# Kernel tuning notes

Measured on AMD Instinct MI355X. Metric: run time of the kernel, lower is better.

The kernel has to match this reference:

```python
import jax, jax.numpy as jnp
import numpy as np

B, S, H = 2, 512, 768
E, M, R, R2 = 64, 64, 128, 128
NER_C, REL_C, SIZE_E, CLS = 10, 8, 32, 101
NEG = -1e30


def _linear(x, w, b):
    # torch nn.Linear convention: w is [out, in]
    return x @ w.T + b


def _span_pool(emb, masks):
    # emb [B,S,H], masks [B,K,S] -> masked max over tokens -> [B,K,H]
    neg = jnp.where(masks[..., None] != 0, 0.0, NEG)  # [B,K,S,1]
    return jnp.max(neg + emb[:, None, :, :], axis=2)


def _classify_spans(input_ids, emb, masks, size_emb, rep_w, rep_b, head_w, head_b):
    pool = _span_pool(emb, masks)                      # [B,K,H]
    cls_idx = jnp.argmax((input_ids == CLS).astype(jnp.int32), axis=1)
    ctx = emb[jnp.arange(emb.shape[0]), cls_idx]       # [B,H] (get_token)
    rep = jnp.concatenate([jnp.broadcast_to(ctx[:, None, :], pool.shape), pool, size_emb], axis=-1)
    clf = _linear(jax.nn.relu(_linear(rep, rep_w, rep_b)), head_w, head_b)
    return clf, pool


def _classify_relations(pool, size_emb, rels, rel_masks, emb, w1, b1, w2, b2, w3, b3):
    Bc = pool.shape[0]
    bidx = jnp.arange(Bc)[:, None, None]
    pairs = pool[bidx, rels].reshape(Bc, rels.shape[1], -1)        # [B,R,2H]
    size_pairs = size_emb[bidx, rels].reshape(Bc, rels.shape[1], -1)  # [B,R,2*SIZE_E]
    # masked max over context tokens (rel mask)
    ctx = jnp.max(jnp.where(rel_masks[..., None] != 0, 0.0, NEG) + emb[:, None, :, :], axis=2)
    ctx = jnp.where(jnp.any(rel_masks != 0, axis=-1)[..., None], ctx, 0.0)
    rel_repr = jnp.concatenate([ctx, pairs, size_pairs], axis=-1)  # [B,R,3H+2*SIZE_E]
    h = jax.nn.relu(_linear(rel_repr, w1, b1))
    h = jax.nn.relu(_linear(h, w2, b2))
    return _linear(h, w3, b3)


def setup_inputs():
    key = jax.random.key(0)
    ks = jax.random.split(key, 24)
    p = lambda k, shape: jax.random.normal(k, shape, jnp.float32) * 0.02
    ids = jax.random.randint(ks[0], (B, S), 2000, 30000)
    ids = ids.at[:, 0].set(CLS)  # exactly one cls token per row
    return dict(
        input_ids=ids,
        entity_masks=jax.random.randint(ks[1], (B, E, S), 0, 2).astype(jnp.int32),
        entity_sizes=jax.random.randint(ks[2], (B, E), 0, 100),
        mention_masks=jax.random.randint(ks[3], (B, M, S), 0, 2).astype(jnp.int32),
        mention_sizes=jax.random.randint(ks[4], (B, M), 0, 100),
        relations=jax.random.randint(ks[5], (B, R, 2), 0, E),
        rel_masks=jax.random.randint(ks[6], (B, R, S), 0, 2).astype(jnp.int32),
        references=jax.random.randint(ks[7], (B, R2, 2), 0, M),
        references_masks=jax.random.randint(ks[8], (B, R2, S), 0, 2).astype(jnp.int32),
        token_embedding=jax.random.normal(ks[9], (B, S, H), jnp.float32),
        ner_size_emb=p(ks[10], (100, SIZE_E)),
        emd_size_emb=p(ks[11], (100, SIZE_E)),
        ner_rep_w=p(ks[12], (H, 2 * H + SIZE_E)), ner_rep_b=jnp.zeros(H, jnp.float32),
        ner_head_w=p(ks[13], (NER_C, H)), ner_head_b=jnp.zeros(NER_C, jnp.float32),
        emd_rep_w=p(ks[14], (H, 2 * H + SIZE_E)), emd_rep_b=jnp.zeros(H, jnp.float32),
        emd_head_w=p(ks[15], (2, H)), emd_head_b=jnp.zeros(2, jnp.float32),
        rel_w1=p(ks[16], (H, 3 * H + 2 * SIZE_E)), rel_b1=jnp.zeros(H, jnp.float32),
        rel_w2=p(ks[17], (H, H)), rel_b2=jnp.zeros(H, jnp.float32),
        rel_w3=p(ks[18], (REL_C, H)), rel_b3=jnp.zeros(REL_C, jnp.float32),
        cr_w1=p(ks[19], (H, 3 * H + 2 * SIZE_E)), cr_b1=jnp.zeros(H, jnp.float32),
        cr_w2=p(ks[20], (H, H)), cr_b2=jnp.zeros(H, jnp.float32),
        cr_w3=p(ks[21], (1, H)), cr_b3=jnp.zeros(1, jnp.float32),
    )


def reference(input_ids, entity_masks, entity_sizes, mention_masks, mention_sizes,
              relations, rel_masks, references, references_masks, token_embedding,
              ner_size_emb, emd_size_emb,
              ner_rep_w, ner_rep_b, ner_head_w, ner_head_b,
              emd_rep_w, emd_rep_b, emd_head_w, emd_head_b,
              rel_w1, rel_b1, rel_w2, rel_b2, rel_w3, rel_b3,
              cr_w1, cr_b1, cr_w2, cr_b2, cr_w3, cr_b3):
    sz = ner_size_emb[entity_sizes]                                    # [B,E,SIZE_E]
    entity_clf, entity_pool = _classify_spans(input_ids, token_embedding, entity_masks, sz,
                                              ner_rep_w, ner_rep_b, ner_head_w, ner_head_b)
    rel_clf = _classify_relations(entity_pool, sz, relations, rel_masks, token_embedding,
                                  rel_w1, rel_b1, rel_w2, rel_b2, rel_w3, rel_b3)
    msz = emd_size_emb[mention_sizes]
    mention_clf, mention_pool = _classify_spans(input_ids, token_embedding, mention_masks, msz,
                                                emd_rep_w, emd_rep_b, emd_head_w, emd_head_b)
    ref_clf = _classify_relations(mention_pool, msz, references, references_masks, token_embedding,
                                  cr_w1, cr_b1, cr_w2, cr_b2, cr_w3, cr_b3)
    return entity_clf, rel_clf, mention_clf, ref_clf
```

## Files before the change

### kernel.cpp

```cpp
#include <hip/hip_runtime.h>
#include <hip/hip_bf16.h>

typedef __hip_bfloat16 bf16;
typedef __attribute__((ext_vector_type(8))) short short8;
typedef __attribute__((ext_vector_type(4))) float f32x4;

#define SS 512
#define HD 768
#define NEGC (-1e30f)
#define NSPLIT 8
#define TOK 64
#define POOL_BLOCKS 768
#define D1_BLOCKS (POOL_BLOCKS + 4)

__device__ __forceinline__ short8 cvt8(float4 a, float4 b)
{
  union { bf16 h[8]; short8 s; } u;
  u.h[0] = __hip_bfloat16(a.x); u.h[1] = __hip_bfloat16(a.y);
  u.h[2] = __hip_bfloat16(a.z); u.h[3] = __hip_bfloat16(a.w);
  u.h[4] = __hip_bfloat16(b.x); u.h[5] = __hip_bfloat16(b.y);
  u.h[6] = __hip_bfloat16(b.z); u.h[7] = __hip_bfloat16(b.w);
  return u.s;
}

__global__ __launch_bounds__(256) void k_d1(
    const int* __restrict__ e_masks, const int* __restrict__ m_masks,
    const int* __restrict__ r_masks, const int* __restrict__ c_masks,
    const float* __restrict__ emb, const int* __restrict__ input_ids,
    const int* __restrict__ esizes, const int* __restrict__ msizes,
    const float* __restrict__ nsemb, const float* __restrict__ esemb,
    bf16* __restrict__ part, int* __restrict__ flags,
    bf16* __restrict__ sze, bf16* __restrict__ szm,
    bf16* __restrict__ ctxb, float* __restrict__ out)
{
  int bx = blockIdx.x;
  int t  = threadIdx.x;

  if (bx >= POOL_BLOCKS) {
    int q = bx - POOL_BLOCKS;
    if (q == 0) {
      for (int i = t; i < 128 * 32; i += 256)
        sze[i] = __hip_bfloat16(nsemb[(size_t)esizes[i >> 5] * 32 + (i & 31)]);
    } else if (q == 1) {
      for (int i = t; i < 128 * 32; i += 256)
        szm[i] = __hip_bfloat16(esemb[(size_t)msizes[i >> 5] * 32 + (i & 31)]);
    } else if (q == 2) {
      __shared__ int s_cls;
      for (int b2 = 0; b2 < 2; b2++) {
        if (t == 0) s_cls = SS;
        __syncthreads();
        for (int s = t; s < SS; s += 256)
          if (input_ids[b2 * SS + s] == 101) atomicMin(&s_cls, s);
        __syncthreads();
        int ci = (s_cls == SS) ? 0 : s_cls;
        for (int hh = t; hh < HD; hh += 256)
          ctxb[(size_t)b2 * HD + hh] = __hip_bfloat16(emb[((size_t)b2 * SS + ci) * HD + hh]);
        __syncthreads();
      }
    } else {
      for (int i = t; i < 3840; i += 256) out[i] = 0.f;
    }
    return;
  }

  int g  = bx % 48;
  int b  = (bx / 48) & 1;
  int sp = bx / 96;
  int j0 = g * 8;

  const int* marr; int row0;
  if      (j0 < 64)  { marr = e_masks; row0 = b*64  +  j0;        }
  else if (j0 < 128) { marr = m_masks; row0 = b*64  + (j0-64);    }
  else if (j0 < 256) { marr = r_masks; row0 = b*128 + (j0-128);   }
  else               { marr = c_masks; row0 = b*128 + (j0-256);   }

  __shared__ unsigned s_pack[TOK];
  __shared__ unsigned s_any;
  if (t == 0) s_any = 0u;
  __syncthreads();

  int sbase = sp * TOK;
  if (t < TOK) {
    unsigned w = 0;
    #pragma unroll
    for (int k = 0; k < 8; k++) {
      int mm = marr[(size_t)(row0 + k) * SS + sbase + t];
      w |= (mm != 0 ? 1u : 0u) << k;
    }
    s_pack[t] = w;
    atomicOr(&s_any, w);
  }
  __syncthreads();

  float a0[8], a1[8], a2[8];
  #pragma unroll
  for (int k = 0; k < 8; k++) { a0[k] = -INFINITY; a1[k] = -INFINITY; a2[k] = -INFINITY; }

  const float* ep = emb + ((size_t)b * SS + sbase) * HD + t * 3;
  #pragma unroll 2
  for (int s = 0; s < TOK; s += 2) {
    float u0 = ep[0];
    float u1 = ep[1];
    float u2 = ep[2];
    float v0 = ep[HD];
    float v1 = ep[HD + 1];
    float v2 = ep[HD + 2];
    ep += 2 * HD;
    unsigned w0 = (unsigned)__builtin_amdgcn_readfirstlane((int)s_pack[s]);
    unsigned w1 = (unsigned)__builtin_amdgcn_readfirstlane((int)s_pack[s + 1]);
    #pragma unroll
    for (int k = 0; k < 8; k++) {
      float add0 = (w0 & (1u << k)) ? 0.f : NEGC;
      float add1 = (w1 & (1u << k)) ? 0.f : NEGC;
      a0[k] = fmaxf(fmaxf(a0[k], u0 + add0), v0 + add1);
      a1[k] = fmaxf(fmaxf(a1[k], u1 + add0), v1 + add1);
      a2[k] = fmaxf(fmaxf(a2[k], u2 + add0), v2 + add1);
    }
  }

  #pragma unroll
  for (int k = 0; k < 8; k++) {
    int sg = b * 384 + j0 + k;
    bf16* dst = part + ((size_t)sg * NSPLIT + sp) * HD + t * 3;
    dst[0] = __hip_bfloat16(a0[k]);
    dst[1] = __hip_bfloat16(a1[k]);
    dst[2] = __hip_bfloat16(a2[k]);
  }
  if (t < 8) flags[(size_t)(b * 384 + j0 + t) * NSPLIT + sp] = (int)((s_any >> t) & 1u);
}

__global__ __launch_bounds__(256) void k_combine(
    const bf16* __restrict__ part, const int* __restrict__ flags,
    bf16* __restrict__ epool, bf16* __restrict__ mpool,
    bf16* __restrict__ rctx, bf16* __restrict__ cctx)
{
  int sg = blockIdx.x;
  int b = sg / 384, j = sg % 384;
  int any = 0;
  #pragma unroll
  for (int sp = 0; sp < NSPLIT; sp++) any |= flags[(size_t)sg * NSPLIT + sp];

  int h = threadIdx.x * 3;
  float v0 = -INFINITY, v1 = -INFINITY, v2 = -INFINITY;
  #pragma unroll
  for (int sp = 0; sp < NSPLIT; sp++) {
    const bf16* src = part + ((size_t)sg * NSPLIT + sp) * HD + h;
    v0 = fmaxf(v0, (float)src[0]);
    v1 = fmaxf(v1, (float)src[1]);
    v2 = fmaxf(v2, (float)src[2]);
  }
  bf16* dst;
  if      (j < 64)  { dst = epool + ((size_t)b*64  + j)       * HD + h; }
  else if (j < 128) { dst = mpool + ((size_t)b*64  + (j-64))  * HD + h; }
  else if (j < 256) { dst = rctx  + ((size_t)b*128 + (j-128)) * HD + h;
                      if (!any) { v0 = 0.f; v1 = 0.f; v2 = 0.f; } }
  else              { dst = cctx  + ((size_t)b*128 + (j-256)) * HD + h;
                      if (!any) { v0 = 0.f; v1 = 0.f; v2 = 0.f; } }
  dst[0] = __hip_bfloat16(v0);
  dst[1] = __hip_bfloat16(v1);
  dst[2] = __hip_bfloat16(v2);
}

struct P1 {
  const bf16 *ctx, *pool, *sz; const int* ridx;
  const float* W; const float* bias;
  bf16* C;
  const float *hw, *hb; float* outp;
  int is_rel, N, K, Mtiles;
};
struct P1x4 { P1 p[4]; };

__global__ __launch_bounds__(256, 2) void k_gemm1(P1x4 args)
{
  P1 g = args.p[blockIdx.z];
  int x = blockIdx.x;
  if (x >= g.Mtiles) return;
  int mt = x * 32, nt = blockIdx.y * 32;
  int wave = threadIdx.x >> 6, lane = threadIdx.x & 63;
  int lm = lane & 15, quad = lane >> 4;
  int K_ = g.K;

  const bf16 *g0[2], *g1[2], *g2[2], *g3[2], *g4[2];
  int rr[2] = { mt + lm, mt + 16 + lm };
  #pragma unroll
  for (int i = 0; i < 2; i++) {
    int r = rr[i];
    if (g.is_rel) {
      int b = r >> 7;
      int i0 = g.ridx[2 * r], i1 = g.ridx[2 * r + 1];
      g0[i] = g.ctx  + (size_t)r * HD;
      g1[i] = g.pool + (size_t)(b * 64 + i0) * HD;
      g2[i] = g.pool + (size_t)(b * 64 + i1) * HD;
      g3[i] = g.sz   + (size_t)(b * 64 + i0) * 32;
      g4[i] = g.sz   + (size_t)(b * 64 + i1) * 32;
    } else {
      g0[i] = g.ctx  + (size_t)(r >> 6) * HD;
      g1[i] = g.pool + (size_t)r * HD;
      g2[i] = g.sz   + (size_t)r * 32;
      g3[i] = g2[i]; g4[i] = g2[i];
    }
  }
  const float* w0p = g.W + (size_t)(nt + lm)      * K_ + quad * 8;
  const float* w1p = g.W + (size_t)(nt + 16 + lm) * K_ + quad * 8;

  f32x4 acc00 = {0.f,0.f,0.f,0.f}, acc01 = {0.f,0.f,0.f,0.f};
  f32x4 acc10 = {0.f,0.f,0.f,0.f}, acc11 = {0.f,0.f,0.f,0.f};

  for (int k32 = wave * 32; k32 < K_; k32 += 128) {
    const bf16 *b0, *b1;
    if      (k32 < 768)  { b0 = g0[0] + k32;          b1 = g0[1] + k32;          }
    else if (k32 < 1536) { b0 = g1[0] + (k32 - 768);  b1 = g1[1] + (k32 - 768);  }
    else if (k32 < 2304) { b0 = g2[0] + (k32 - 1536); b1 = g2[1] + (k32 - 1536); }
    else if (k32 < 2336) { b0 = g3[0] + (k32 - 2304); b1 = g3[1] + (k32 - 2304); }
    else                 { b0 = g4[0] + (k32 - 2336); b1 = g4[1] + (k32 - 2336); }
    short8 a0 = *(const short8*)((const short*)b0 + quad * 8);
    short8 a1 = *(const short8*)((const short*)b1 + quad * 8);
    const float* wq0 = w0p + k32;
    const float* wq1 = w1p + k32;
    short8 w0 = cvt8(*(const float4*)wq0, *(const float4*)(wq0 + 4));
    short8 w1 = cvt8(*(const float4*)wq1, *(const float4*)(wq1 + 4));
    acc00 = __builtin_amdgcn_mfma_f32_16x16x32_bf16(a0, w0, acc00, 0, 0, 0);
    acc01 = __builtin_amdgcn_mfma_f32_16x16x32_bf16(a0, w1, acc01, 0, 0, 0);
    acc10 = __builtin_amdgcn_mfma_f32_16x16x32_bf16(a1, w0, acc10, 0, 0, 0);
    acc11 = __builtin_amdgcn_mfma_f32_16x16x32_bf16(a1, w1, acc11, 0, 0, 0);
  }

  __shared__ float smem[4 * 32 * 32];
  #pragma unroll
  for (int reg = 0; reg < 4; reg++) {
    int r = quad * 4 + reg;
    smem[wave*1024 + r*32 + lm]             = acc00[reg];
    smem[wave*1024 + r*32 + 16 + lm]        = acc01[reg];
    smem[wave*1024 + (16 + r)*32 + lm]      = acc10[reg];
    smem[wave*1024 + (16 + r)*32 + 16 + lm] = acc11[reg];
  }
  __syncthreads();

  int c = threadIdx.x & 31;
  int rb = threadIdx.x >> 5;
  float bb = g.bias[nt + c];
  #pragma unroll
  for (int i = 0; i < 4; i++) {
    int r = rb + 8 * i;
    float v = smem[r*32 + c] + smem[1024 + r*32 + c] + smem[2048 + r*32 + c] + smem[3072 + r*32 + c];
    v = fmaxf(v + bb, 0.f);
    if (g.C) g.C[(size_t)(mt + r) * HD + nt + c] = __hip_bfloat16(v);
    else     smem[r*32 + c] = v;
  }
  __syncthreads();

  if (!g.C) {
    int r = threadIdx.x >> 3, oi = threadIdx.x & 7;
    for (int o = oi; o < g.N; o += 8) {
      float s = 0.f;
      #pragma unroll
      for (int cc = 0; cc < 32; cc++) {
        int c2 = (cc + r) & 31;
        s += smem[r*32 + c2] * g.hw[(size_t)o * HD + nt + c2];
      }
      if (blockIdx.y == 0) s += g.hb[o];
      atomicAdd(g.outp + (size_t)(mt + r) * g.N + o, s);
    }
  }
}

struct P2 { const short* A; const float* W; const float* bias;
            const float *hw, *hb; float* outp; int N; };
struct P2x2 { P2 p[2]; };

__global__ __launch_bounds__(256, 2) void k_gemm2(P2x2 args)
{
  P2 g = args.p[blockIdx.z];
  int mt = blockIdx.x * 32, nt = blockIdx.y * 32;
  int wave = threadIdx.x >> 6, lane = threadIdx.x & 63;
  int lm = lane & 15, quad = lane >> 4;

  const short* a0p = g.A + (size_t)(mt + lm)      * HD + quad * 8;
  const short* a1p = g.A + (size_t)(mt + 16 + lm) * HD + quad * 8;
  const float* w0p = g.W + (size_t)(nt + lm)      * HD + quad * 8;
  const float* w1p = g.W + (size_t)(nt + 16 + lm) * HD + quad * 8;

  f32x4 acc00 = {0.f,0.f,0.f,0.f}, acc01 = {0.f,0.f,0.f,0.f};
  f32x4 acc10 = {0.f,0.f,0.f,0.f}, acc11 = {0.f,0.f,0.f,0.f};

  for (int k32 = wave * 32; k32 < HD; k32 += 128) {
    short8 a0 = *(const short8*)(a0p + k32);
    short8 a1 = *(const short8*)(a1p + k32);
    short8 w0 = cvt8(*(const float4*)(w0p + k32), *(const float4*)(w0p + k32 + 4));
    short8 w1 = cvt8(*(const float4*)(w1p + k32), *(const float4*)(w1p + k32 + 4));
    acc00 = __builtin_amdgcn_mfma_f32_16x16x32_bf16(a0, w0, acc00, 0, 0, 0);
    acc01 = __builtin_amdgcn_mfma_f32_16x16x32_bf16(a0, w1, acc01, 0, 0, 0);
    acc10 = __builtin_amdgcn_mfma_f32_16x16x32_bf16(a1, w0, acc10, 0, 0, 0);
    acc11 = __builtin_amdgcn_mfma_f32_16x16x32_bf16(a1, w1, acc11, 0, 0, 0);
  }

  __shared__ float smem[4 * 32 * 32];
  #pragma unroll
  for (int reg = 0; reg < 4; reg++) {
    int r = quad * 4 + reg;
    smem[wave*1024 + r*32 + lm]             = acc00[reg];
    smem[wave*1024 + r*32 + 16 + lm]        = acc01[reg];
    smem[wave*1024 + (16 + r)*32 + lm]      = acc10[reg];
    smem[wave*1024 + (16 + r)*32 + 16 + lm] = acc11[reg];
  }
  __syncthreads();

  int c = threadIdx.x & 31;
  int rb = threadIdx.x >> 5;
  float bb = g.bias[nt + c];
  #pragma unroll
  for (int i = 0; i < 4; i++) {
    int r = rb + 8 * i;
    float v = smem[r*32 + c] + smem[1024 + r*32 + c] + smem[2048 + r*32 + c] + smem[3072 + r*32 + c];
    smem[r*32 + c] = fmaxf(v + bb, 0.f);
  }
  __syncthreads();

  int r = threadIdx.x >> 3, oi = threadIdx.x & 7;
  for (int o = oi; o < g.N; o += 8) {
    float s = 0.f;
    #pragma unroll
    for (int cc = 0; cc < 32; cc++) {
      int c2 = (cc + r) & 31;
      s += smem[r*32 + c2] * g.hw[(size_t)o * HD + nt + c2];
    }
    if (blockIdx.y == 0) s += g.hb[o];
    atomicAdd(g.outp + (size_t)(mt + r) * g.N + o, s);
  }
}

extern "C" void kernel_launch(void* const* d_in, const int* in_sizes, int n_in,
                              void* d_out, int out_size, void* d_ws, size_t ws_size,
                              hipStream_t stream)
{
  const int*   input_ids  = (const int*)d_in[0];
  const int*   e_masks    = (const int*)d_in[1];
  const int*   e_sizes    = (const int*)d_in[2];
  const int*   m_masks    = (const int*)d_in[3];
  const int*   m_sizes    = (const int*)d_in[4];
  const int*   relations  = (const int*)d_in[5];
  const int*   r_masks    = (const int*)d_in[6];
  const int*   references = (const int*)d_in[7];
  const int*   c_masks    = (const int*)d_in[8];
  const float* emb        = (const float*)d_in[9];
  const float* nsemb      = (const float*)d_in[10];
  const float* esemb      = (const float*)d_in[11];
  const float* ner_rep_w  = (const float*)d_in[12];
  const float* ner_rep_b  = (const float*)d_in[13];
  const float* ner_head_w = (const float*)d_in[14];
  const float* ner_head_b = (const float*)d_in[15];
  const float* emd_rep_w  = (const float*)d_in[16];
  const float* emd_rep_b  = (const float*)d_in[17];
  const float* emd_head_w = (const float*)d_in[18];
  const float* emd_head_b = (const float*)d_in[19];
  const float* rel_w1 = (const float*)d_in[20];
  const float* rel_b1 = (const float*)d_in[21];
  const float* rel_w2 = (const float*)d_in[22];
  const float* rel_b2 = (const float*)d_in[23];
  const float* rel_w3 = (const float*)d_in[24];
  const float* rel_b3 = (const float*)d_in[25];
  const float* cr_w1 = (const float*)d_in[26];
  const float* cr_b1 = (const float*)d_in[27];
  const float* cr_w2 = (const float*)d_in[28];
  const float* cr_b2 = (const float*)d_in[29];
  const float* cr_w3 = (const float*)d_in[30];
  const float* cr_b3 = (const float*)d_in[31];
  float* out = (float*)d_out;

  bf16* wsb = (bf16*)d_ws;
  size_t ob = 0;
  bf16* PART  = wsb + ob; ob += (size_t)NSPLIT * 768 * HD;
  bf16* EPOOL = wsb + ob; ob += (size_t)128 * HD;
  bf16* MPOOL = wsb + ob; ob += (size_t)128 * HD;
  bf16* RCTX  = wsb + ob; ob += (size_t)256 * HD;
  bf16* CCTX  = wsb + ob; ob += (size_t)256 * HD;
  bf16* SZE   = wsb + ob; ob += (size_t)128 * 32;
  bf16* SZM   = wsb + ob; ob += (size_t)128 * 32;
  bf16* CTXB  = wsb + ob; ob += (size_t)2 * HD;
  bf16* RH1   = wsb + ob; ob += (size_t)256 * HD;
  bf16* CH1   = wsb + ob; ob += (size_t)256 * HD;
  int*  FLAGS = (int*)(wsb + ob); ob += (size_t)2 * NSPLIT * 768;

  k_d1<<<D1_BLOCKS, 256, 0, stream>>>(
      e_masks, m_masks, r_masks, c_masks, emb, input_ids,
      e_sizes, m_sizes, nsemb, esemb,
      PART, FLAGS, SZE, SZM, CTXB, out);

  k_combine<<<768, 256, 0, stream>>>(PART, FLAGS, EPOOL, MPOOL, RCTX, CCTX);

  P1x4 a1;
  a1.p[0] = { CTXB, EPOOL, SZE, nullptr,    ner_rep_w, ner_rep_b,
              nullptr, ner_head_w, ner_head_b, out,        0, 10, 1568, 4 };
  a1.p[1] = { CTXB, MPOOL, SZM, nullptr,    emd_rep_w, emd_rep_b,
              nullptr, emd_head_w, emd_head_b, out + 3328, 0, 2,  1568, 4 };
  a1.p[2] = { RCTX, EPOOL, SZE, relations,  rel_w1, rel_b1,
              RH1, nullptr, nullptr, nullptr,              1, 0,  2368, 8 };
  a1.p[3] = { CCTX, MPOOL, SZM, references, cr_w1, cr_b1,
              CH1, nullptr, nullptr, nullptr,              1, 0,  2368, 8 };
  k_gemm1<<<dim3(8, 24, 4), 256, 0, stream>>>(a1);

  P2x2 a2;
  a2.p[0] = { (const short*)RH1, rel_w2, rel_b2, rel_w3, rel_b3, out + 1280, 8 };
  a2.p[1] = { (const short*)CH1, cr_w2,  cr_b2,  cr_w3,  cr_b3,  out + 3584, 1 };
  k_gemm2<<<dim3(8, 24, 2), 256, 0, stream>>>(a2);
}
```

Baseline: 207.3 us.

## Pre-convert GEMM weights to bf16 once inside the pooling kernel

Adds 128 extra blocks to the first (pooling) kernel. They convert all fp32 weight matrices used by the two GEMM kernels into bf16 workspace copies. The GEMMs then load bf16 weights directly instead of converting fp32 to bf16 inside the MFMA loop. This halves weight bytes read by the GEMMs and removes the repeated per-tile conversions, in exchange for one extra fp32-read/bf16-write pass over every weight on each call. The GEMM grids are also flattened to 1D with z-interleaved block ordering, which changes how blocks are scheduled across CUs.

```diff
diff --git a/kernel.cpp b/kernel.cpp
--- a/kernel.cpp
+++ b/kernel.cpp
@@ -11,7 +11,8 @@
 #define NSPLIT 8
 #define TOK 64
 #define POOL_BLOCKS 768
-#define D1_BLOCKS (POOL_BLOCKS + 4)
+#define NCONV 128
+#define D1_BLOCKS (POOL_BLOCKS + 4 + NCONV)
 
 __device__ __forceinline__ short8 cvt8(float4 a, float4 b)
 {
@@ -22,6 +23,9 @@
   u.h[6] = __hip_bfloat16(b.z); u.h[7] = __hip_bfloat16(b.w);
   return u.s;
 }
+
+struct WC { const float* s; bf16* d; int n8; };
+struct WC6 { WC c[6]; };
 
 __global__ __launch_bounds__(256) void k_d1(
     const int* __restrict__ e_masks, const int* __restrict__ m_masks,
@@ -31,7 +35,7 @@
     const float* __restrict__ nsemb, const float* __restrict__ esemb,
     bf16* __restrict__ part, int* __restrict__ flags,
     bf16* __restrict__ sze, bf16* __restrict__ szm,
-    bf16* __restrict__ ctxb, float* __restrict__ out)
+    bf16* __restrict__ ctxb, float* __restrict__ out, WC6 wc)
 {
   int bx = blockIdx.x;
   int t  = threadIdx.x;
@@ -57,8 +61,21 @@
           ctxb[(size_t)b2 * HD + hh] = __hip_bfloat16(emb[((size_t)b2 * SS + ci) * HD + hh]);
         __syncthreads();
       }
+    } else if (q == 3) {
+      for (int i = t; i < 3840; i += 256) out[i] = 0.f;
     } else {
-      for (int i = t; i < 3840; i += 256) out[i] = 0.f;
+      int cid = q - 4;
+      #pragma unroll
+      for (int seg = 0; seg < 6; seg++) {
+        const float* s = wc.c[seg].s;
+        bf16* dp = wc.c[seg].d;
+        int n8 = wc.c[seg].n8;
+        for (int i = cid * 256 + t; i < n8; i += NCONV * 256) {
+          float4 f0 = *(const float4*)(s + (size_t)i * 8);
+          float4 f1 = *(const float4*)(s + (size_t)i * 8 + 4);
+          *(short8*)(dp + (size_t)i * 8) = cvt8(f0, f1);
+        }
+      }
     }
     return;
   }
@@ -163,7 +180,7 @@
 
 struct P1 {
   const bf16 *ctx, *pool, *sz; const int* ridx;
-  const float* W; const float* bias;
+  const bf16* W; const float* bias;
   bf16* C;
   const float *hw, *hb; float* outp;
   int is_rel, N, K, Mtiles;
@@ -172,10 +189,13 @@
 
 __global__ __launch_bounds__(256, 2) void k_gemm1(P1x4 args)
 {
-  P1 g = args.p[blockIdx.z];
-  int x = blockIdx.x;
+  int id = blockIdx.x;
+  int x = id / 96;
+  int r96 = id % 96;
+  int y = r96 % 24, z = r96 / 24;
+  P1 g = args.p[z];
   if (x >= g.Mtiles) return;
-  int mt = x * 32, nt = blockIdx.y * 32;
+  int mt = x * 32, nt = y * 32;
   int wave = threadIdx.x >> 6, lane = threadIdx.x & 63;
   int lm = lane & 15, quad = lane >> 4;
   int K_ = g.K;
@@ -184,24 +204,24 @@
   int rr[2] = { mt + lm, mt + 16 + lm };
   #pragma unroll
   for (int i = 0; i < 2; i++) {
-    int r = rr[i];
+    int rI = rr[i];
     if (g.is_rel) {
-      int b = r >> 7;
-      int i0 = g.ridx[2 * r], i1 = g.ridx[2 * r + 1];
-      g0[i] = g.ctx  + (size_t)r * HD;
+      int b = rI >> 7;
+      int i0 = g.ridx[2 * rI], i1 = g.ridx[2 * rI + 1];
+      g0[i] = g.ctx  + (size_t)rI * HD;
       g1[i] = g.pool + (size_t)(b * 64 + i0) * HD;
       g2[i] = g.pool + (size_t)(b * 64 + i1) * HD;
       g3[i] = g.sz   + (size_t)(b * 64 + i0) * 32;
       g4[i] = g.sz   + (size_t)(b * 64 + i1) * 32;
     } else {
-      g0[i] = g.ctx  + (size_t)(r >> 6) * HD;
-      g1[i] = g.pool + (size_t)r * HD;
-      g2[i] = g.sz   + (size_t)r * 32;
+      g0[i] = g.ctx  + (size_t)(rI >> 6) * HD;
+      g1[i] = g.pool + (size_t)rI * HD;
+      g2[i] = g.sz   + (size_t)rI * 32;
       g3[i] = g2[i]; g4[i] = g2[i];
     }
   }
-  const float* w0p = g.W + (size_t)(nt + lm)      * K_ + quad * 8;
-  const float* w1p = g.W + (size_t)(nt + 16 + lm) * K_ + quad * 8;
+  const bf16* w0p = g.W + (size_t)(nt + lm)      * K_ + quad * 8;
+  const bf16* w1p = g.W + (size_t)(nt + 16 + lm) * K_ + quad * 8;
 
   f32x4 acc00 = {0.f,0.f,0.f,0.f}, acc01 = {0.f,0.f,0.f,0.f};
   f32x4 acc10 = {0.f,0.f,0.f,0.f}, acc11 = {0.f,0.f,0.f,0.f};
@@ -215,10 +235,8 @@
     else                 { b0 = g4[0] + (k32 - 2336); b1 = g4[1] + (k32 - 2336); }
     short8 a0 = *(const short8*)((const short*)b0 + quad * 8);
     short8 a1 = *(const short8*)((const short*)b1 + quad * 8);
-    const float* wq0 = w0p + k32;
-    const float* wq1 = w1p + k32;
-    short8 w0 = cvt8(*(const float4*)wq0, *(const float4*)(wq0 + 4));
-    short8 w1 = cvt8(*(const float4*)wq1, *(const float4*)(wq1 + 4));
+    short8 w0 = *(const short8*)(w0p + k32);
+    short8 w1 = *(const short8*)(w1p + k32);
     acc00 = __builtin_amdgcn_mfma_f32_16x16x32_bf16(a0, w0, acc00, 0, 0, 0);
     acc01 = __builtin_amdgcn_mfma_f32_16x16x32_bf16(a0, w1, acc01, 0, 0, 0);
     acc10 = __builtin_amdgcn_mfma_f32_16x16x32_bf16(a1, w0, acc10, 0, 0, 0);
@@ -228,11 +246,11 @@
   __shared__ float smem[4 * 32 * 32];
   #pragma unroll
   for (int reg = 0; reg < 4; reg++) {
-    int r = quad * 4 + reg;
-    smem[wave*1024 + r*32 + lm]             = acc00[reg];
-    smem[wave*1024 + r*32 + 16 + lm]        = acc01[reg];
-    smem[wave*1024 + (16 + r)*32 + lm]      = acc10[reg];
-    smem[wave*1024 + (16 + r)*32 + 16 + lm] = acc11[reg];
+    int rI = quad * 4 + reg;
+    smem[wave*1024 + rI*32 + lm]             = acc00[reg];
+    smem[wave*1024 + rI*32 + 16 + lm]        = acc01[reg];
+    smem[wave*1024 + (16 + rI)*32 + lm]      = acc10[reg];
+    smem[wave*1024 + (16 + rI)*32 + 16 + lm] = acc11[reg];
   }
   __syncthreads();
 
@@ -241,44 +259,49 @@
   float bb = g.bias[nt + c];
   #pragma unroll
   for (int i = 0; i < 4; i++) {
-    int r = rb + 8 * i;
-    float v = smem[r*32 + c] + smem[1024 + r*32 + c] + smem[2048 + r*32 + c] + smem[3072 + r*32 + c];
+    int rI = rb + 8 * i;
+    float v = smem[rI*32 + c] + smem[1024 + rI*32 + c] + smem[2048 + rI*32 + c] + smem[3072 + rI*32 + c];
     v = fmaxf(v + bb, 0.f);
-    if (g.C) g.C[(size_t)(mt + r) * HD + nt + c] = __hip_bfloat16(v);
-    else     smem[r*32 + c] = v;
+    if (g.C) g.C[(size_t)(mt + rI) * HD + nt + c] = __hip_bfloat16(v);
+    else     smem[rI*32 + c] = v;
   }
   __syncthreads();
 
   if (!g.C) {
-    int r = threadIdx.x >> 3, oi = threadIdx.x & 7;
+    int rI = threadIdx.x >> 3, oi = threadIdx.x & 7;
     for (int o = oi; o < g.N; o += 8) {
       float s = 0.f;
       #pragma unroll
       for (int cc = 0; cc < 32; cc++) {
-        int c2 = (cc + r) & 31;
-        s += smem[r*32 + c2] * g.hw[(size_t)o * HD + nt + c2];
+        int c2 = (cc + rI) & 31;
+        s += smem[rI*32 + c2] * g.hw[(size_t)o * HD + nt + c2];
       }
-      if (blockIdx.y == 0) s += g.hb[o];
-      atomicAdd(g.outp + (size_t)(mt + r) * g.N + o, s);
-    }
-  }
-}
-
-struct P2 { const short* A; const float* W; const float* bias;
+      if (blockIdx.x % 96 < 24) ;
+      if (y == 0) s += g.hb[o];
+      atomicAdd(g.outp + (size_t)(mt + rI) * g.N + o, s);
+    }
+  }
+}
+
+struct P2 { const short* A; const bf16* W; const float* bias;
             const float *hw, *hb; float* outp; int N; };
 struct P2x2 { P2 p[2]; };
 
 __global__ __launch_bounds__(256, 2) void k_gemm2(P2x2 args)
 {
-  P2 g = args.p[blockIdx.z];
-  int mt = blockIdx.x * 32, nt = blockIdx.y * 32;
+  int id = blockIdx.x;
+  int x = id / 48;
+  int r48 = id % 48;
+  int y = r48 % 24, z = r48 / 24;
+  P2 g = args.p[z];
+  int mt = x * 32, nt = y * 32;
   int wave = threadIdx.x >> 6, lane = threadIdx.x & 63;
   int lm = lane & 15, quad = lane >> 4;
 
   const short* a0p = g.A + (size_t)(mt + lm)      * HD + quad * 8;
   const short* a1p = g.A + (size_t)(mt + 16 + lm) * HD + quad * 8;
-  const float* w0p = g.W + (size_t)(nt + lm)      * HD + quad * 8;
-  const float* w1p = g.W + (size_t)(nt + 16 + lm) * HD + quad * 8;
+  const bf16* w0p = g.W + (size_t)(nt + lm)      * HD + quad * 8;
+  const bf16* w1p = g.W + (size_t)(nt + 16 + lm) * HD + quad * 8;
 
   f32x4 acc00 = {0.f,0.f,0.f,0.f}, acc01 = {0.f,0.f,0.f,0.f};
   f32x4 acc10 = {0.f,0.f,0.f,0.f}, acc11 = {0.f,0.f,0.f,0.f};
@@ -286,8 +309,8 @@
   for (int k32 = wave * 32; k32 < HD; k32 += 128) {
     short8 a0 = *(const short8*)(a0p + k32);
     short8 a1 = *(const short8*)(a1p + k32);
-    short8 w0 = cvt8(*(const float4*)(w0p + k32), *(const float4*)(w0p + k32 + 4));
-    short8 w1 = cvt8(*(const float4*)(w1p + k32), *(const float4*)(w1p + k32 + 4));
+    short8 w0 = *(const short8*)(w0p + k32);
+    short8 w1 = *(const short8*)(w1p + k32);
     acc00 = __builtin_amdgcn_mfma_f32_16x16x32_bf16(a0, w0, acc00, 0, 0, 0);
     acc01 = __builtin_amdgcn_mfma_f32_16x16x32_bf16(a0, w1, acc01, 0, 0, 0);
     acc10 = __builtin_amdgcn_mfma_f32_16x16x32_bf16(a1, w0, acc10, 0, 0, 0);
@@ -297,11 +320,11 @@
   __shared__ float smem[4 * 32 * 32];
   #pragma unroll
   for (int reg = 0; reg < 4; reg++) {
-    int r = quad * 4 + reg;
-    smem[wave*1024 + r*32 + lm]             = acc00[reg];
-    smem[wave*1024 + r*32 + 16 + lm]        = acc01[reg];
-    smem[wave*1024 + (16 + r)*32 + lm]      = acc10[reg];
-    smem[wave*1024 + (16 + r)*32 + 16 + lm] = acc11[reg];
+    int rI = quad * 4 + reg;
+    smem[wave*1024 + rI*32 + lm]             = acc00[reg];
+    smem[wave*1024 + rI*32 + 16 + lm]        = acc01[reg];
+    smem[wave*1024 + (16 + rI)*32 + lm]      = acc10[reg];
+    smem[wave*1024 + (16 + rI)*32 + 16 + lm] = acc11[reg];
   }
   __syncthreads();
 
@@ -310,22 +333,22 @@
   float bb = g.bias[nt + c];
   #pragma unroll
   for (int i = 0; i < 4; i++) {
-    int r = rb + 8 * i;
-    float v = smem[r*32 + c] + smem[1024 + r*32 + c] + smem[2048 + r*32 + c] + smem[3072 + r*32 + c];
-    smem[r*32 + c] = fmaxf(v + bb, 0.f);
-  }
-  __syncthreads();
-
-  int r = threadIdx.x >> 3, oi = threadIdx.x & 7;
+    int rI = rb + 8 * i;
+    float v = smem[rI*32 + c] + smem[1024 + rI*32 + c] + smem[2048 + rI*32 + c] + smem[3072 + rI*32 + c];
+    smem[rI*32 + c] = fmaxf(v + bb, 0.f);
+  }
+  __syncthreads();
+
+  int rI = threadIdx.x >> 3, oi = threadIdx.x & 7;
   for (int o = oi; o < g.N; o += 8) {
     float s = 0.f;
     #pragma unroll
     for (int cc = 0; cc < 32; cc++) {
-      int c2 = (cc + r) & 31;
-      s += smem[r*32 + c2] * g.hw[(size_t)o * HD + nt + c2];
-    }
-    if (blockIdx.y == 0) s += g.hb[o];
-    atomicAdd(g.outp + (size_t)(mt + r) * g.N + o, s);
+      int c2 = (cc + rI) & 31;
+      s += smem[rI*32 + c2] * g.hw[(size_t)o * HD + nt + c2];
+    }
+    if (y == 0) s += g.hb[o];
+    atomicAdd(g.outp + (size_t)(mt + rI) * g.N + o, s);
   }
 }
 
@@ -380,27 +403,41 @@
   bf16* RH1   = wsb + ob; ob += (size_t)256 * HD;
   bf16* CH1   = wsb + ob; ob += (size_t)256 * HD;
   int*  FLAGS = (int*)(wsb + ob); ob += (size_t)2 * NSPLIT * 768;
+  bf16* WB_NER = wsb + ob; ob += (size_t)HD * 1568;
+  bf16* WB_EMD = wsb + ob; ob += (size_t)HD * 1568;
+  bf16* WB_RW1 = wsb + ob; ob += (size_t)HD * 2368;
+  bf16* WB_CW1 = wsb + ob; ob += (size_t)HD * 2368;
+  bf16* WB_RW2 = wsb + ob; ob += (size_t)HD * HD;
+  bf16* WB_CW2 = wsb + ob; ob += (size_t)HD * HD;
+
+  WC6 wc;
+  wc.c[0] = { ner_rep_w, WB_NER, HD * 1568 / 8 };
+  wc.c[1] = { emd_rep_w, WB_EMD, HD * 1568 / 8 };
+  wc.c[2] = { rel_w1,    WB_RW1, HD * 2368 / 8 };
+  wc.c[3] = { cr_w1,     WB_CW1, HD * 2368 / 8 };
+  wc.c[4] = { rel_w2,    WB_RW2, HD * HD / 8 };
+  wc.c[5] = { cr_w2,     WB_CW2, HD * HD / 8 };
 
   k_d1<<<D1_BLOCKS, 256, 0, stream>>>(
       e_masks, m_masks, r_masks, c_masks, emb, input_ids,
       e_sizes, m_sizes, nsemb, esemb,
-      PART, FLAGS, SZE, SZM, CTXB, out);
+      PART, FLAGS, SZE, SZM, CTXB, out, wc);
 
   k_combine<<<768, 256, 0, stream>>>(PART, FLAGS, EPOOL, MPOOL, RCTX, CCTX);
 
   P1x4 a1;
-  a1.p[0] = { CTXB, EPOOL, SZE, nullptr,    ner_rep_w, ner_rep_b,
+  a1.p[0] = { CTXB, EPOOL, SZE, nullptr,    WB_NER, ner_rep_b,
               nullptr, ner_head_w, ner_head_b, out,        0, 10, 1568, 4 };
-  a1.p[1] = { CTXB, MPOOL, SZM, nullptr,    emd_rep_w, emd_rep_b,
+  a1.p[1] = { CTXB, MPOOL, SZM, nullptr,    WB_EMD, emd_rep_b,
               nullptr, emd_head_w, emd_head_b, out + 3328, 0, 2,  1568, 4 };
-  a1.p[2] = { RCTX, EPOOL, SZE, relations,  rel_w1, rel_b1,
+  a1.p[2] = { RCTX, EPOOL, SZE, relations,  WB_RW1, rel_b1,
               RH1, nullptr, nullptr, nullptr,              1, 0,  2368, 8 };
-  a1.p[3] = { CCTX, MPOOL, SZM, references, cr_w1, cr_b1,
+  a1.p[3] = { CCTX, MPOOL, SZM, references, WB_CW1, cr_b1,
               CH1, nullptr, nullptr, nullptr,              1, 0,  2368, 8 };
-  k_gemm1<<<dim3(8, 24, 4), 256, 0, stream>>>(a1);
+  k_gemm1<<<8 * 96, 256, 0, stream>>>(a1);
 
   P2x2 a2;
-  a2.p[0] = { (const short*)RH1, rel_w2, rel_b2, rel_w3, rel_b3, out + 1280, 8 };
-  a2.p[1] = { (const short*)CH1, cr_w2,  cr_b2,  cr_w3,  cr_b3,  out + 3584, 1 };
-  k_gemm2<<<dim3(8, 24, 2), 256, 0, stream>>>(a2);
-}
+  a2.p[0] = { (const short*)RH1, WB_RW2, rel_b2, rel_w3, rel_b3, out + 1280, 8 };
+  a2.p[1] = { (const short*)CH1, WB_CW2, cr_b2,  cr_w3,  cr_b3,  out + 3584, 1 };
+  k_gemm2<<<8 * 48, 256, 0, stream>>>(a2);
+}
```

Result: faster. 190.7 us (-8.0%).
